# Performance work log

Measured on AMD Instinct MI355X. Metric: run time of the kernel, lower is better.

## Reference

```python
import jax, jax.numpy as jnp
import numpy as np

N_HEAD = 16


def setup_inputs() -> dict:
    key = jax.random.key(0)
    ks = jax.random.split(key, 6)
    B, T, C = 2, 2048, 1024
    x = jax.random.normal(ks[0], (B, T, C), dtype=jnp.float32)
    mask = jnp.ones((B, T), dtype=jnp.int32)
    s = 1.0 / np.sqrt(C)
    Wqkv = jax.random.normal(ks[1], (C, 3 * C), dtype=jnp.float32) * s
    bqkv = jax.random.normal(ks[2], (3 * C,), dtype=jnp.float32) * 0.02
    Wproj = jax.random.normal(ks[3], (C, C), dtype=jnp.float32) * s
    bproj = jax.random.normal(ks[4], (C,), dtype=jnp.float32) * 0.02
    return {"x": x, "mask": mask, "Wqkv": Wqkv, "bqkv": bqkv,
            "Wproj": Wproj, "bproj": bproj}


def reference(x, mask, Wqkv, bqkv, Wproj, bproj):
    B, T, C = x.shape
    H = N_HEAD
    Dh = C // H
    scale = 1.0 / np.sqrt(Dh)
    qkv = x @ Wqkv + bqkv                       # [B,T,3C]
    q, k, v = jnp.split(qkv, 3, axis=-1)
    # [B,T,C] -> [B,H,T,Dh]
    q = q.reshape(B, T, H, Dh).transpose(0, 2, 1, 3)
    k = k.reshape(B, T, H, Dh).transpose(0, 2, 1, 3)
    v = v.reshape(B, T, H, Dh).transpose(0, 2, 1, 3)
    attn = jnp.einsum('bhid,bhjd->bhij', q, k) * scale  # [B,H,T,T]
    m = mask[:, None, None, :]                  # b j -> b 1 1 j
    attn = jnp.where(m == 0, -jnp.inf, attn)
    attn = jax.nn.softmax(attn, axis=-1)
    y = jnp.einsum('bhij,bhjd->bhid', attn, v)  # [B,H,T,Dh]
    y = y.transpose(0, 2, 1, 3).reshape(B, T, C)
    return y @ Wproj + bproj
```

## Files before the change

kernel.cpp:

```cpp
#include <hip/hip_runtime.h>

using US   = unsigned short;
using bf8  = __attribute__((ext_vector_type(8))) __bf16;
using us8  = __attribute__((ext_vector_type(8))) US;
using us4  = __attribute__((ext_vector_type(4))) US;
using f4   = __attribute__((ext_vector_type(4))) float;
using f8   = __attribute__((ext_vector_type(8))) float;
using f16v = __attribute__((ext_vector_type(16))) float;
using i4   = __attribute__((ext_vector_type(4))) int;
using u2   = __attribute__((ext_vector_type(2))) unsigned;

__device__ __forceinline__ US f2bf(float x) {
  union { float f; unsigned u; } v; v.f = x;
  unsigned r = v.u + 0x7fffu + ((v.u >> 16) & 1u);
  return (US)(r >> 16);
}
__device__ __forceinline__ unsigned cvtpk(float a, float b) {
  unsigned r;
  asm("v_cvt_pk_bf16_f32 %0, %1, %2" : "=v"(r) : "v"(a), "v"(b));
  return r;
}
#if __has_builtin(__builtin_amdgcn_exp2f)
__device__ __forceinline__ float ex2(float x) { return __builtin_amdgcn_exp2f(x); }
#else
__device__ __forceinline__ float ex2(float x) {
  float r;
  asm("v_exp_f32 %0, %1" : "=v"(r) : "v"(x));
  return r;
}
#endif
__device__ __forceinline__ void gl16(const US* g, US* l) {
  __builtin_amdgcn_global_load_lds((const __attribute__((address_space(1))) void*)g,
                                   (__attribute__((address_space(3))) void*)l, 16, 0, 0);
}

__global__ void cvt_k(const float* __restrict__ in, US* __restrict__ out, int n8) {
  int i = blockIdx.x * blockDim.x + threadIdx.x;
  if (i >= n8) return;
  f8 v = ((const f8*)in)[i];
  us8 o;
#pragma unroll
  for (int j = 0; j < 8; ++j) o[j] = f2bf(v[j]);
  ((us8*)out)[i] = o;
}

__global__ void trw_k(const float* __restrict__ in, US* __restrict__ out, int R, int C) {
  __shared__ float tile[32][33];
  int bx = blockIdx.x * 32, by = blockIdx.y * 32;
  int tx = threadIdx.x & 31, ty = threadIdx.x >> 5;
  for (int i = ty; i < 32; i += 8)
    tile[i][tx] = in[(size_t)(by + i) * C + bx + tx];
  __syncthreads();
  for (int i = ty; i < 32; i += 8)
    out[(size_t)(bx + i) * R + by + tx] = f2bf(tile[tx][i]);
}

__device__ __forceinline__ int SW4(int row) { return (row & 3) ^ ((row >> 2) & 3); }

template <typename OT, bool QSC = false, bool VT = false>
__global__ __launch_bounds__(256, 2) void gemm_ct(const US* __restrict__ A,
                                                  const US* __restrict__ Bt,
                                                  const float* __restrict__ bias,
                                                  OT* __restrict__ out,
                                                  US* __restrict__ vtout,
                                                  int M, int N, int K) {
  __shared__ US lA[3][128 * 32];
  __shared__ US lB[3][128 * 32];
  const int t = threadIdx.x;
  const int lane = t & 63;
  const int w = t >> 6;
  const int wr = w >> 1, wc = w & 1;
  const int l15 = lane & 15, g = lane >> 4;
  const int m0 = blockIdx.x * 128, n0 = blockIdx.y * 128;

  float bv[4];
#pragma unroll
  for (int ni = 0; ni < 4; ++ni)
    bv[ni] = bias ? bias[n0 + wc * 64 + ni * 16 + l15] : 0.0f;

  const int r16 = lane >> 2;
  const int u4 = lane & 3;
  const int csw = (u4 ^ SW4(r16)) * 8;

#define GSTAGE(buf, k0s)                                                          \
  {                                                                               \
    _Pragma("unroll") for (int s = 0; s < 2; ++s) {                               \
      const int rb = w * 32 + s * 16;                                             \
      gl16(A + (size_t)(m0 + rb + r16) * K + (k0s) + csw, &lA[buf][rb * 32]);     \
      gl16(Bt + (size_t)(n0 + rb + r16) * K + (k0s) + csw, &lB[buf][rb * 32]);    \
    }                                                                             \
  }

  GSTAGE(0, 0);

  f4 acc[4][4] = {};
  const int kk = K >> 5;
  int cur = 0;
  for (int tt = 0; tt < kk; ++tt) {
    if (tt + 1 < kk) {
      int nb = cur + 1; if (nb == 3) nb = 0;
      GSTAGE(nb, (tt + 1) * 32);
      asm volatile("s_waitcnt vmcnt(4)" ::: "memory");
    } else {
      asm volatile("s_waitcnt vmcnt(0)" ::: "memory");
    }
    __builtin_amdgcn_s_barrier();
    asm volatile("" ::: "memory");

    const US* a_ = lA[cur];
    const US* b_ = lB[cur];
    bf8 af[4], bfr[4];
#pragma unroll
    for (int mi = 0; mi < 4; ++mi) {
      int row = wr * 64 + mi * 16 + l15;
      af[mi] = *(const bf8*)((const char*)a_ + row * 64 + ((g ^ SW4(row)) << 4));
    }
#pragma unroll
    for (int ni = 0; ni < 4; ++ni) {
      int row = wc * 64 + ni * 16 + l15;
      bfr[ni] = *(const bf8*)((const char*)b_ + row * 64 + ((g ^ SW4(row)) << 4));
    }
    __builtin_amdgcn_s_setprio(1);
#pragma unroll
    for (int mi = 0; mi < 4; ++mi)
#pragma unroll
      for (int ni = 0; ni < 4; ++ni)
        acc[mi][ni] = __builtin_amdgcn_mfma_f32_16x16x32_bf16(af[mi], bfr[ni], acc[mi][ni], 0, 0, 0);
    __builtin_amdgcn_s_setprio(0);
    cur = cur + 1 == 3 ? 0 : cur + 1;
  }
#undef GSTAGE

  if (VT && n0 >= 2048) {
#pragma unroll
    for (int ni = 0; ni < 4; ++ni) {
      int cv = n0 - 2048 + wc * 64 + ni * 16 + l15;
      int h2 = cv >> 6, d = cv & 63;
#pragma unroll
      for (int mi = 0; mi < 4; ++mi) {
        int rowb = m0 + wr * 64 + mi * 16 + g * 4;
        int bb = rowb >> 11, tloc = rowb & 2047;
        us4 pk;
#pragma unroll
        for (int r = 0; r < 4; ++r) pk[r] = f2bf(acc[mi][ni][r] + bv[ni]);
        *(us4*)(vtout + ((size_t)(bb * 16 + h2) * 64 + d) * 2048 + tloc) = pk;
      }
    }
    return;
  }
  const float oscale = (QSC && n0 < 1024) ? 0.18033688011f : 1.0f;
#pragma unroll
  for (int ni = 0; ni < 4; ++ni) {
    int col = n0 + wc * 64 + ni * 16 + l15;
#pragma unroll
    for (int mi = 0; mi < 4; ++mi) {
      int rowb = m0 + wr * 64 + mi * 16 + g * 4;
#pragma unroll
      for (int r = 0; r < 4; ++r) {
        float val = (acc[mi][ni][r] + bv[ni]) * oscale;
        if constexpr (sizeof(OT) == 2)
          out[(size_t)(rowb + r) * N + col] = f2bf(val);
        else
          out[(size_t)(rowb + r) * N + col] = val;
      }
    }
  }
}

__device__ __forceinline__ const bf8* fragp(const US* base, int r, int ks, int hi) {
  int byte = r * 128 + ((((ks << 1) | hi) ^ (r & 7)) << 4);
  return (const bf8*)((const char*)base + byte);
}

__global__ __launch_bounds__(256, 2) void attn_k(const US* __restrict__ qkv,
                                                 const US* __restrict__ vt,
                                                 const int* __restrict__ mask,
                                                 US* __restrict__ y) {
  int f0 = blockIdx.x;
  int f = ((f0 & 7) << 6) | (f0 >> 3);
  const int qt = f & 15;
  const int bh = f >> 4;
  const int b = bh >> 4;
  const int h = bh & 15;
  const int lane = threadIdx.x & 63, w = threadIdx.x >> 6;
  const int l31 = lane & 31, hi = lane >> 5;

  __shared__ US lK[4][64 * 64];
  __shared__ US lV[4][64 * 64];
  __shared__ unsigned char lMaskB[256];

  const int qr0 = qt * 128 + w * 32;
  const US* qrow = qkv + (size_t)(b * 2048 + qr0 + l31) * 3072 + h * 64 + hi * 8;
  bf8 qf[4];
#pragma unroll
  for (int ks = 0; ks < 4; ++ks) qf[ks] = *(const bf8*)(qrow + ks * 16);

  const int r8 = lane >> 3;
  const int c16 = (lane & 7) ^ r8;
  const US* kg = qkv + (size_t)b * 2048 * 3072 + 1024 + h * 64 + c16 * 8;
  const US* vg = vt + (size_t)bh * 64 * 2048 + c16 * 8;
  const int R0 = w * 16;

  f16v o0 = {}, o1 = {};
  f16v osum = {};
  bf8 pf[4] = {};
  bf8 ones;
  {
    union { US u[8]; bf8 v; } on;
#pragma unroll
    for (int i = 0; i < 8; ++i) on.u[i] = 0x3F80;
    ones = on.v;
  }

#define STAGE(buf, j0s)                                                        \
  {                                                                            \
    gl16(kg + (size_t)((j0s) + R0 + r8) * 3072, &lK[buf][R0 * 64]);            \
    gl16(kg + (size_t)((j0s) + R0 + 8 + r8) * 3072, &lK[buf][(R0 + 8) * 64]);  \
    gl16(vg + (size_t)(R0 + r8) * 2048 + (j0s), &lV[buf][R0 * 64]);            \
    gl16(vg + (size_t)(R0 + 8 + r8) * 2048 + (j0s), &lV[buf][(R0 + 8) * 64]);  \
  }

  STAGE(0, 0);

  int allones;
  {
    const int t8 = threadIdx.x * 8;
    i4 ma = *(const i4*)(mask + b * 2048 + t8);
    i4 mc = *(const i4*)(mask + b * 2048 + t8 + 4);
    unsigned byte = 0;
#pragma unroll
    for (int k = 0; k < 4; ++k) {
      byte |= (ma[k] != 0 ? 1u : 0u) << k;
      byte |= (mc[k] != 0 ? 1u : 0u) << (k + 4);
    }
    lMaskB[threadIdx.x] = (unsigned char)byte;
    allones = __syncthreads_and((int)(byte == 0xFFu));
  }

#pragma unroll 4
  for (int tt = 0; tt < 32; ++tt) {
    const int cur = tt & 3;
    const int j0 = tt * 64;
    if (tt < 31) {
      STAGE((tt + 1) & 3, j0 + 64);
      asm volatile("s_waitcnt vmcnt(4)" ::: "memory");
    } else {
      asm volatile("s_waitcnt vmcnt(0)" ::: "memory");
    }
    __builtin_amdgcn_s_barrier();
    asm volatile("" ::: "memory");

    const US* lKc = lK[cur];

    f16v s0 = {}, s1 = {};
    __builtin_amdgcn_s_setprio(1);
#pragma unroll
    for (int ks = 0; ks < 4; ++ks) {
      bf8 ka0 = *fragp(lKc, l31, ks, hi);
      bf8 ka1 = *fragp(lKc, 32 + l31, ks, hi);
      s0 = __builtin_amdgcn_mfma_f32_32x32x16_bf16(ka0, qf[ks], s0, 0, 0, 0);
      s1 = __builtin_amdgcn_mfma_f32_32x32x16_bf16(ka1, qf[ks], s1, 0, 0, 0);
    }
    if (tt) {
      const US* lVp = lV[(tt + 3) & 3];
#pragma unroll
      for (int ks = 0; ks < 4; ++ks) {
        bf8 vf0 = *fragp(lVp, l31, ks, hi);
        bf8 vf1 = *fragp(lVp, 32 + l31, ks, hi);
        o0 = __builtin_amdgcn_mfma_f32_32x32x16_bf16(vf0, pf[ks], o0, 0, 0, 0);
        o1 = __builtin_amdgcn_mfma_f32_32x32x16_bf16(vf1, pf[ks], o1, 0, 0, 0);
        osum = __builtin_amdgcn_mfma_f32_32x32x16_bf16(ones, pf[ks], osum, 0, 0, 0);
      }
    }
    __builtin_amdgcn_s_setprio(0);

#pragma unroll
    for (int i = 0; i < 16; ++i) {
      s0[i] = ex2(s0[i]);
      s1[i] = ex2(s1[i]);
    }
    if (!allones) {
      unsigned mbyte = lMaskB[(j0 >> 3) + (lane >> 3)];
      int mword = (mbyte >> (lane & 7)) & 1;
      unsigned long long mbits = __ballot(mword != 0);
#pragma unroll
      for (int i = 0; i < 16; ++i) {
        int r = (i & 3) + 8 * (i >> 2) + 4 * hi;
        if (!((mbits >> r) & 1)) s0[i] = 0.0f;
        if (!((mbits >> (32 + r)) & 1)) s1[i] = 0.0f;
      }
    }

#pragma unroll
    for (int ks = 0; ks < 4; ++ks) {
      const f16v& st = (ks < 2) ? s0 : s1;
      const int R = (ks & 1) * 8;
      unsigned w0 = cvtpk(st[R + 0], st[R + 1]);
      unsigned w1 = cvtpk(st[R + 2], st[R + 3]);
      unsigned w2 = cvtpk(st[R + 4], st[R + 5]);
      unsigned w3 = cvtpk(st[R + 6], st[R + 7]);
      u2 p02 = __builtin_amdgcn_permlane32_swap(w0, w2, false, false);
      u2 p13 = __builtin_amdgcn_permlane32_swap(w1, w3, false, false);
      union { unsigned u[4]; bf8 v; } bld;
      bld.u[0] = p02[0];
      bld.u[1] = p13[0];
      bld.u[2] = p02[1];
      bld.u[3] = p13[1];
      pf[ks] = bld.v;
    }
  }
#undef STAGE

  {
    const US* lVp = lV[3];
    __builtin_amdgcn_s_setprio(1);
#pragma unroll
    for (int ks = 0; ks < 4; ++ks) {
      bf8 vf0 = *fragp(lVp, l31, ks, hi);
      bf8 vf1 = *fragp(lVp, 32 + l31, ks, hi);
      o0 = __builtin_amdgcn_mfma_f32_32x32x16_bf16(vf0, pf[ks], o0, 0, 0, 0);
      o1 = __builtin_amdgcn_mfma_f32_32x32x16_bf16(vf1, pf[ks], o1, 0, 0, 0);
      osum = __builtin_amdgcn_mfma_f32_32x32x16_bf16(ones, pf[ks], osum, 0, 0, 0);
    }
    __builtin_amdgcn_s_setprio(0);
  }

  float inv = 1.0f / osum[0];
  US* yrow = y + (size_t)(b * 2048 + qr0 + l31) * 1024 + h * 64;
#pragma unroll
  for (int qd = 0; qd < 4; ++qd) {
    us4 pk0, pk1;
#pragma unroll
    for (int j = 0; j < 4; ++j) {
      pk0[j] = f2bf(o0[qd * 4 + j] * inv);
      pk1[j] = f2bf(o1[qd * 4 + j] * inv);
    }
    *(us4*)(yrow + qd * 8 + hi * 4) = pk0;
    *(us4*)(yrow + 32 + qd * 8 + hi * 4) = pk1;
  }
}

extern "C" void kernel_launch(void* const* d_in, const int* in_sizes, int n_in,
                              void* d_out, int out_size, void* d_ws, size_t ws_size,
                              hipStream_t stream) {
  const float* x     = (const float*)d_in[0];
  const int*   mask  = (const int*)d_in[1];
  const float* Wqkv  = (const float*)d_in[2];
  const float* bqkv  = (const float*)d_in[3];
  const float* Wproj = (const float*)d_in[4];
  const float* bproj = (const float*)d_in[5];
  float* out = (float*)d_out;

  US* xb     = (US*)d_ws;
  US* qkvb   = xb     + (size_t)4096 * 1024;
  US* WqkvT  = qkvb   + (size_t)4096 * 3072;
  US* WprojT = WqkvT  + (size_t)3072 * 1024;
  US* Vt     = WprojT + (size_t)1024 * 1024;
  US* yb     = Vt     + (size_t)32 * 64 * 2048;

  cvt_k<<<2048, 256, 0, stream>>>(x, xb, 4096 * 1024 / 8);
  trw_k<<<dim3(96, 32), 256, 0, stream>>>(Wqkv, WqkvT, 1024, 3072);
  trw_k<<<dim3(32, 32), 256, 0, stream>>>(Wproj, WprojT, 1024, 1024);
  gemm_ct<US, true, true><<<dim3(32, 24), 256, 0, stream>>>(xb, WqkvT, bqkv, qkvb, Vt, 4096, 3072, 1024);
  attn_k<<<512, 256, 0, stream>>>(qkvb, Vt, mask, yb);
  gemm_ct<float><<<dim3(32, 8), 256, 0, stream>>>(yb, WprojT, bproj, out, nullptr, 4096, 1024, 1024);
}
```

Before: 116.9 us.

## Drop software-pipelined PV stage and shrink LDS ring to three buffers

Replaces the skewed loop, in which the P·V MFMAs for the previous tile overlapped the QK^T of the current tile, with a non-skewed per-tile sequence: QK^T, exp and mask, pack, then P·V on the same tile. This frees the fourth K/V LDS buffer, so the ring becomes three buffers unrolled by three with constant indices, lowering LDS use and the live pf registers. It gives up the MFMA/exp overlap inside a wave, relying on the second co-resident workgroup to hide the dependency chain.

```diff
diff --git a/kernel.cpp b/kernel.cpp
--- a/kernel.cpp
+++ b/kernel.cpp
@@ -185,8 +185,8 @@
   const int lane = threadIdx.x & 63, w = threadIdx.x >> 6;
   const int l31 = lane & 31, hi = lane >> 5;
 
-  __shared__ US lK[4][64 * 64];
-  __shared__ US lV[4][64 * 64];
+  __shared__ US lK[3][64 * 64];
+  __shared__ US lV[3][64 * 64];
   __shared__ unsigned char lMaskB[256];
 
   const int qr0 = qt * 128 + w * 32;
@@ -203,7 +203,6 @@
 
   f16v o0 = {}, o1 = {};
   f16v osum = {};
-  bf8 pf[4] = {};
   bf8 ones;
   {
     union { US u[8]; bf8 v; } on;
@@ -237,93 +236,80 @@
     allones = __syncthreads_and((int)(byte == 0xFFu));
   }
 
-#pragma unroll 4
-  for (int tt = 0; tt < 32; ++tt) {
-    const int cur = tt & 3;
-    const int j0 = tt * 64;
-    if (tt < 31) {
-      STAGE((tt + 1) & 3, j0 + 64);
-      asm volatile("s_waitcnt vmcnt(4)" ::: "memory");
-    } else {
-      asm volatile("s_waitcnt vmcnt(0)" ::: "memory");
-    }
-    __builtin_amdgcn_s_barrier();
-    asm volatile("" ::: "memory");
-
-    const US* lKc = lK[cur];
-
-    f16v s0 = {}, s1 = {};
-    __builtin_amdgcn_s_setprio(1);
-#pragma unroll
-    for (int ks = 0; ks < 4; ++ks) {
-      bf8 ka0 = *fragp(lKc, l31, ks, hi);
-      bf8 ka1 = *fragp(lKc, 32 + l31, ks, hi);
-      s0 = __builtin_amdgcn_mfma_f32_32x32x16_bf16(ka0, qf[ks], s0, 0, 0, 0);
-      s1 = __builtin_amdgcn_mfma_f32_32x32x16_bf16(ka1, qf[ks], s1, 0, 0, 0);
-    }
-    if (tt) {
-      const US* lVp = lV[(tt + 3) & 3];
-#pragma unroll
-      for (int ks = 0; ks < 4; ++ks) {
-        bf8 vf0 = *fragp(lVp, l31, ks, hi);
-        bf8 vf1 = *fragp(lVp, 32 + l31, ks, hi);
-        o0 = __builtin_amdgcn_mfma_f32_32x32x16_bf16(vf0, pf[ks], o0, 0, 0, 0);
-        o1 = __builtin_amdgcn_mfma_f32_32x32x16_bf16(vf1, pf[ks], o1, 0, 0, 0);
-        osum = __builtin_amdgcn_mfma_f32_32x32x16_bf16(ones, pf[ks], osum, 0, 0, 0);
-      }
-    }
-    __builtin_amdgcn_s_setprio(0);
-
-#pragma unroll
-    for (int i = 0; i < 16; ++i) {
-      s0[i] = ex2(s0[i]);
-      s1[i] = ex2(s1[i]);
-    }
-    if (!allones) {
-      unsigned mbyte = lMaskB[(j0 >> 3) + (lane >> 3)];
-      int mword = (mbyte >> (lane & 7)) & 1;
-      unsigned long long mbits = __ballot(mword != 0);
-#pragma unroll
-      for (int i = 0; i < 16; ++i) {
-        int r = (i & 3) + 8 * (i >> 2) + 4 * hi;
-        if (!((mbits >> r) & 1)) s0[i] = 0.0f;
-        if (!((mbits >> (32 + r)) & 1)) s1[i] = 0.0f;
-      }
-    }
-
-#pragma unroll
-    for (int ks = 0; ks < 4; ++ks) {
-      const f16v& st = (ks < 2) ? s0 : s1;
-      const int R = (ks & 1) * 8;
-      unsigned w0 = cvtpk(st[R + 0], st[R + 1]);
-      unsigned w1 = cvtpk(st[R + 2], st[R + 3]);
-      unsigned w2 = cvtpk(st[R + 4], st[R + 5]);
-      unsigned w3 = cvtpk(st[R + 6], st[R + 7]);
-      u2 p02 = __builtin_amdgcn_permlane32_swap(w0, w2, false, false);
-      u2 p13 = __builtin_amdgcn_permlane32_swap(w1, w3, false, false);
-      union { unsigned u[4]; bf8 v; } bld;
-      bld.u[0] = p02[0];
-      bld.u[1] = p13[0];
-      bld.u[2] = p02[1];
-      bld.u[3] = p13[1];
-      pf[ks] = bld.v;
-    }
-  }
+#define ATILE(tt, CUR, NXT, LAST)                                              \
+  {                                                                            \
+    const int j0_ = (tt) * 64;                                                 \
+    if (!(LAST)) {                                                             \
+      STAGE(NXT, j0_ + 64);                                                    \
+      asm volatile("s_waitcnt vmcnt(4)" ::: "memory");                         \
+    } else {                                                                   \
+      asm volatile("s_waitcnt vmcnt(0)" ::: "memory");                         \
+    }                                                                          \
+    __builtin_amdgcn_s_barrier();                                              \
+    asm volatile("" ::: "memory");                                             \
+    const US* lKc = lK[CUR];                                                   \
+    const US* lVc = lV[CUR];                                                   \
+    f16v s0 = {}, s1 = {};                                                     \
+    __builtin_amdgcn_s_setprio(1);                                             \
+    _Pragma("unroll") for (int ks = 0; ks < 4; ++ks) {                         \
+      bf8 ka0 = *fragp(lKc, l31, ks, hi);                                      \
+      bf8 ka1 = *fragp(lKc, 32 + l31, ks, hi);                                 \
+      s0 = __builtin_amdgcn_mfma_f32_32x32x16_bf16(ka0, qf[ks], s0, 0, 0, 0);  \
+      s1 = __builtin_amdgcn_mfma_f32_32x32x16_bf16(ka1, qf[ks], s1, 0, 0, 0);  \
+    }                                                                          \
+    __builtin_amdgcn_s_setprio(0);                                             \
+    _Pragma("unroll") for (int i = 0; i < 16; ++i) {                           \
+      s0[i] = ex2(s0[i]);                                                      \
+      s1[i] = ex2(s1[i]);                                                      \
+    }                                                                          \
+    if (!allones) {                                                            \
+      unsigned mbyte = lMaskB[(j0_ >> 3) + (lane >> 3)];                       \
+      int mword = (mbyte >> (lane & 7)) & 1;                                   \
+      unsigned long long mbits = __ballot(mword != 0);                         \
+      _Pragma("unroll") for (int i = 0; i < 16; ++i) {                         \
+        int r = (i & 3) + 8 * (i >> 2) + 4 * hi;                               \
+        if (!((mbits >> r) & 1)) s0[i] = 0.0f;                                 \
+        if (!((mbits >> (32 + r)) & 1)) s1[i] = 0.0f;                          \
+      }                                                                        \
+    }                                                                          \
+    bf8 pf[4];                                                                 \
+    _Pragma("unroll") for (int ks = 0; ks < 4; ++ks) {                         \
+      const f16v& st = (ks < 2) ? s0 : s1;                                     \
+      const int R = (ks & 1) * 8;                                              \
+      unsigned w0 = cvtpk(st[R + 0], st[R + 1]);                               \
+      unsigned w1 = cvtpk(st[R + 2], st[R + 3]);                               \
+      unsigned w2 = cvtpk(st[R + 4], st[R + 5]);                               \
+      unsigned w3 = cvtpk(st[R + 6], st[R + 7]);                               \
+      u2 p02 = __builtin_amdgcn_permlane32_swap(w0, w2, false, false);         \
+      u2 p13 = __builtin_amdgcn_permlane32_swap(w1, w3, false, false);         \
+      union { unsigned u[4]; bf8 v; } bld;                                     \
+      bld.u[0] = p02[0];                                                       \
+      bld.u[1] = p13[0];                                                       \
+      bld.u[2] = p02[1];                                                       \
+      bld.u[3] = p13[1];                                                       \
+      pf[ks] = bld.v;                                                          \
+    }                                                                          \
+    __builtin_amdgcn_s_setprio(1);                                             \
+    _Pragma("unroll") for (int ks = 0; ks < 4; ++ks) {                         \
+      bf8 vf0 = *fragp(lVc, l31, ks, hi);                                      \
+      bf8 vf1 = *fragp(lVc, 32 + l31, ks, hi);                                 \
+      o0 = __builtin_amdgcn_mfma_f32_32x32x16_bf16(vf0, pf[ks], o0, 0, 0, 0);  \
+      o1 = __builtin_amdgcn_mfma_f32_32x32x16_bf16(vf1, pf[ks], o1, 0, 0, 0);  \
+      osum = __builtin_amdgcn_mfma_f32_32x32x16_bf16(ones, pf[ks], osum, 0, 0, 0); \
+    }                                                                          \
+    __builtin_amdgcn_s_setprio(0);                                             \
+  }
+
+  for (int gg = 0; gg < 10; ++gg) {
+    const int t3 = gg * 3;
+    ATILE(t3, 0, 1, 0)
+    ATILE(t3 + 1, 1, 2, 0)
+    ATILE(t3 + 2, 2, 0, 0)
+  }
+  ATILE(30, 0, 1, 0)
+  ATILE(31, 1, 2, 1)
+#undef ATILE
 #undef STAGE
-
-  {
-    const US* lVp = lV[3];
-    __builtin_amdgcn_s_setprio(1);
-#pragma unroll
-    for (int ks = 0; ks < 4; ++ks) {
-      bf8 vf0 = *fragp(lVp, l31, ks, hi);
-      bf8 vf1 = *fragp(lVp, 32 + l31, ks, hi);
-      o0 = __builtin_amdgcn_mfma_f32_32x32x16_bf16(vf0, pf[ks], o0, 0, 0, 0);
-      o1 = __builtin_amdgcn_mfma_f32_32x32x16_bf16(vf1, pf[ks], o1, 0, 0, 0);
-      osum = __builtin_amdgcn_mfma_f32_32x32x16_bf16(ones, pf[ks], osum, 0, 0, 0);
-    }
-    __builtin_amdgcn_s_setprio(0);
-  }
 
   float inv = 1.0f / osum[0];
   US* yrow = y + (size_t)(b * 2048 + qr0 + l31) * 1024 + h * 64;
```

After: 117.6 us. No clear change (+0.6%).
